# Optimization experiments

Hardware: AMD Instinct MI355X
Metric: run time of the kernel (lower is better)

The kernel has to match this reference:

```python
import jax, jax.numpy as jnp
import numpy as np

B, S, H, NH = 4, 2048, 768, 12
HD = H // NH

def _ln(x, g, b, eps=1e-5):
    m = jnp.mean(x, -1, keepdims=True)
    v = jnp.mean((x - m) ** 2, -1, keepdims=True)
    return (x - m) * jax.lax.rsqrt(v + eps) * g + b

def setup_inputs() -> dict:
    key = jax.random.key(0)
    ks = jax.random.split(key, 16)
    s = 0.02
    return {
        "x": jax.random.normal(ks[0], (B, S, H), jnp.float32),
        "prev_state": jax.random.normal(ks[1], (B, S, H), jnp.float32),
        "mask": jax.random.randint(ks[2], (B,), 0, 2).astype(bool),
        # depthwise conv1d (groups=H, k=3): torch weight [H, 1, 3] == OIH
        "conv_dw_w": jax.random.normal(ks[3], (H, 1, 3), jnp.float32) * s,
        "conv_dw_b": jnp.zeros((H,), jnp.float32),
        # pointwise conv1d (k=1) stored as [out, in]
        "conv_pw_w": jax.random.normal(ks[4], (H, H), jnp.float32) * s,
        "conv_pw_b": jnp.zeros((H,), jnp.float32),
        "cn_g": jnp.ones((H,), jnp.float32), "cn_b": jnp.zeros((H,), jnp.float32),
        "Wq": jax.random.normal(ks[5], (H, H), jnp.float32) * s, "bq": jnp.zeros((H,), jnp.float32),
        "Wk": jax.random.normal(ks[6], (H, H), jnp.float32) * s, "bk": jnp.zeros((H,), jnp.float32),
        "Wv": jax.random.normal(ks[7], (H, H), jnp.float32) * s, "bv": jnp.zeros((H,), jnp.float32),
        "Wo": jax.random.normal(ks[8], (H, H), jnp.float32) * s, "bo": jnp.zeros((H,), jnp.float32),
        "pn_g": jnp.ones((H,), jnp.float32), "pn_b": jnp.zeros((H,), jnp.float32),
        "Wpost": jax.random.normal(ks[9], (H, H), jnp.float32) * s, "bpost": jnp.zeros((H,), jnp.float32),
        "Wg": jax.random.normal(ks[10], (1, 2 * H), jnp.float32) * s, "bg": jnp.zeros((1,), jnp.float32),
    }

def reference(x, prev_state, mask, conv_dw_w, conv_dw_b, conv_pw_w, conv_pw_b,
              cn_g, cn_b, Wq, bq, Wk, bk, Wv, bv, Wo, bo,
              pn_g, pn_b, Wpost, bpost, Wg, bg):
    # ---- bridge: depthwise conv (k=3) -> pointwise conv (k=1) -> GELU -> LN ----
    mem_t = prev_state.transpose(0, 2, 1)  # [B, H, S]
    dw = jax.lax.conv_general_dilated(
        mem_t, conv_dw_w, window_strides=(1,), padding=[(1, 1)],
        feature_group_count=H, dimension_numbers=("NCH", "OIH", "NCH")) + conv_dw_b[None, :, None]
    pw = jnp.einsum("bhs,oh->bos", dw, conv_pw_w) + conv_pw_b[None, :, None]
    bridged = jax.nn.gelu(pw, approximate=False).transpose(0, 2, 1)  # [B, S, H]
    bridged = _ln(bridged, cn_g, cn_b)
    # ---- cross attention: q from x, k/v from bridged memory (nope, non-causal) ----
    q = (jnp.einsum("bsh,oh->bso", x, Wq) + bq).reshape(B, S, NH, HD)
    k = (jnp.einsum("bsh,oh->bso", bridged, Wk) + bk).reshape(B, S, NH, HD)
    v = (jnp.einsum("bsh,oh->bso", bridged, Wv) + bv).reshape(B, S, NH, HD)
    scores = jnp.einsum("bqnd,bknd->bnqk", q, k) / np.float32(np.sqrt(HD))
    attn = jax.nn.softmax(scores, axis=-1)
    ao = jnp.einsum("bnqk,bknd->bqnd", attn, v).reshape(B, S, H)
    ao = jnp.einsum("bsh,oh->bso", ao, Wo) + bo
    # ---- post-attn norm, linear, gate, scatter-add back under mask ----
    inj = _ln(ao, pn_g, pn_b)
    inj = jnp.einsum("bsh,oh->bso", inj, Wpost) + bpost
    gate = jax.nn.sigmoid(jnp.einsum("bsh,oh->bso", jnp.concatenate([x, bridged], -1), Wg) + bg)
    gated = gate * jnp.tanh(inj)
    mf = mask.astype(x.dtype)[:, None, None]  # batch-row select == masked scatter-add
    out = x + mf * gated
    # masked MSE aux loss (only over selected rows, as in the original)
    denom = jnp.maximum(mask.sum(), 1).astype(x.dtype) * np.float32(S * H)
    aux = jnp.sum(mf * (bridged - x) ** 2) / denom
    return out, aux
```

## Files before the change

kernel.cpp:

```cpp
#include <hip/hip_runtime.h>
#include <math.h>

#define B_ 4
#define S_ 2048
#define H_ 768
#define NH_ 12
#define HD_ 64
#define BSH (B_ * S_ * H_)
#define NROWS (B_ * S_)
#define WSZ (H_ * H_)

typedef __attribute__((ext_vector_type(8))) short bf16x8;
typedef __attribute__((ext_vector_type(4))) short s16x4;
typedef __attribute__((ext_vector_type(4))) float f32x4;
typedef __attribute__((ext_vector_type(2))) unsigned u32x2;
typedef __attribute__((ext_vector_type(4))) unsigned u32x4;

__device__ __forceinline__ short f2bf(float f) {
  union { float f; unsigned u; } x; x.f = f;
  unsigned r = x.u + 0x7FFF + ((x.u >> 16) & 1);
  return (short)(r >> 16);
}
__device__ __forceinline__ float bf2f(short s) {
  union { unsigned u; float f; } x;
  x.u = ((unsigned)(unsigned short)s) << 16;
  return x.f;
}
__device__ __forceinline__ unsigned bfpack(float lo, float hi) {
  union { float f; unsigned u; } a, b; a.f = lo; b.f = hi;
  return __builtin_amdgcn_perm(b.u, a.u, 0x07060302);
}

__device__ __forceinline__ void plswap32(unsigned& a, unsigned& b) {
#if __has_builtin(__builtin_amdgcn_permlane32_swap)
  u32x2 r = __builtin_amdgcn_permlane32_swap(a, b, false, false);
  a = r.x; b = r.y;
#else
  asm volatile("v_permlane32_swap_b32 %0, %1" : "+v"(a), "+v"(b));
#endif
}
__device__ __forceinline__ void plswap16(unsigned& a, unsigned& b) {
#if __has_builtin(__builtin_amdgcn_permlane16_swap)
  u32x2 r = __builtin_amdgcn_permlane16_swap(a, b, false, false);
  a = r.x; b = r.y;
#else
  asm volatile("v_permlane16_swap_b32 %0, %1" : "+v"(a), "+v"(b));
#endif
}

typedef __attribute__((address_space(1))) const unsigned int g_u32;
typedef __attribute__((address_space(3))) unsigned int l_u32;
__device__ __forceinline__ void gload16(const void* g, void* l) {
  __builtin_amdgcn_global_load_lds((g_u32*)g, (l_u32*)l, 16, 0, 0);
}

__global__ __launch_bounds__(256) void cvt_x_k(const float* __restrict__ src,
                                               short* __restrict__ dst) {
  int i = (blockIdx.x * 256 + threadIdx.x) * 4;
  float4 v = *(const float4*)(src + i);
  s16x4 o = {f2bf(v.x), f2bf(v.y), f2bf(v.z), f2bf(v.w)};
  *(s16x4*)(dst + i) = o;
}

__global__ __launch_bounds__(256) void cvt6_k(const float* w0, const float* w1,
                                              const float* w2, const float* w3,
                                              const float* w4, const float* w5,
                                              short* __restrict__ dst) {
  int i = (blockIdx.x * 256 + threadIdx.x) * 4;
  int m = i / WSZ;
  int off = i - m * WSZ;
  const float* s = m == 0 ? w0 : m == 1 ? w1 : m == 2 ? w2 : m == 3 ? w3 : m == 4 ? w4 : w5;
  float sc = (m == 1) ? 0.1803368802f : 1.0f;
  float4 v = *(const float4*)(s + off);
  s16x4 o = {f2bf(v.x * sc), f2bf(v.y * sc), f2bf(v.z * sc), f2bf(v.w * sc)};
  *(s16x4*)(dst + i) = o;
}

__global__ __launch_bounds__(192) void dwconv_k(const float* __restrict__ prev,
                                                const float* __restrict__ w3,
                                                const float* __restrict__ bias,
                                                short* __restrict__ out) {
  int row = blockIdx.x;
  int s = row & (S_ - 1);
  int h = threadIdx.x * 4;
  size_t base = (size_t)row * H_ + h;
  float4 c = *(const float4*)(prev + base);
  float4 wa = *(const float4*)(w3 + h * 3);
  float4 wb = *(const float4*)(w3 + h * 3 + 4);
  float4 wc = *(const float4*)(w3 + h * 3 + 8);
  float4 bi = *(const float4*)(bias + h);
  float4 acc;
  acc.x = bi.x + c.x * wa.y;
  acc.y = bi.y + c.y * wb.x;
  acc.z = bi.z + c.z * wb.w;
  acc.w = bi.w + c.w * wc.z;
  if (s > 0) {
    float4 l = *(const float4*)(prev + base - H_);
    acc.x += l.x * wa.x; acc.y += l.y * wa.w; acc.z += l.z * wb.z; acc.w += l.w * wc.y;
  }
  if (s < S_ - 1) {
    float4 r = *(const float4*)(prev + base + H_);
    acc.x += r.x * wa.z; acc.y += r.y * wb.y; acc.z += r.z * wc.x; acc.w += r.w * wc.w;
  }
  s16x4 o = {f2bf(acc.x), f2bf(acc.y), f2bf(acc.z), f2bf(acc.w)};
  *(s16x4*)(out + base) = o;
}

struct GemmJob {
  const short* A; const short* W; const float* bias; short* C; int act; int tout;
  float bscale;
};

__global__ __launch_bounds__(256) void gemm_bf2(GemmJob j0, GemmJob j1, GemmJob j2) {
  int d = blockIdx.x;
  int z = d / 384, r5 = d - z * 384;
  GemmJob j = z == 0 ? j0 : (z == 1 ? j1 : j2);
  int xcd = r5 & 7, s5 = r5 >> 3;
  int nx = s5 % 6, ny = xcd + 8 * (s5 / 6);
  __shared__ short As[128 * 64];
  __shared__ short Ws[128 * 64];
  int tid = threadIdx.x, lane = tid & 63, w = tid >> 6;
  int wr = w >> 1, wc = w & 1, lm = lane & 15, lq = lane >> 4;
  int m0 = ny * 128, n0 = nx * 128;
  int srow = lane >> 3;
  int skc = (lane & 7) * 8;
  const short* gA = j.A + (size_t)(m0 + w * 32 + srow) * H_ + skc;
  const short* gW = j.W + (size_t)(n0 + w * 32 + srow) * H_ + skc;
  short* lA = As + w * 2048;
  short* lW = Ws + w * 2048;

  f32x4 acc[4][4];
#pragma unroll
  for (int i = 0; i < 4; ++i)
#pragma unroll
    for (int jj = 0; jj < 4; ++jj) acc[i][jj] = (f32x4){0.f, 0.f, 0.f, 0.f};

  for (int kt = 0; kt < H_; kt += 64) {
    __syncthreads();
#pragma unroll
    for (int c = 0; c < 4; ++c) {
      gload16(gA + kt + (size_t)(c * 8) * H_, lA + c * 512);
      gload16(gW + kt + (size_t)(c * 8) * H_, lW + c * 512);
    }
    __syncthreads();
#pragma unroll
    for (int kk = 0; kk < 2; ++kk) {
      bf16x8 af[4], wf[4];
#pragma unroll
      for (int i = 0; i < 4; ++i)
        af[i] = *(const bf16x8*)&As[(wr * 64 + i * 16 + lm) * 64 + kk * 32 + lq * 8];
#pragma unroll
      for (int jj = 0; jj < 4; ++jj)
        wf[jj] = *(const bf16x8*)&Ws[(wc * 64 + jj * 16 + lm) * 64 + kk * 32 + lq * 8];
#pragma unroll
      for (int i = 0; i < 4; ++i)
#pragma unroll
        for (int jj = 0; jj < 4; ++jj)
          acc[i][jj] = __builtin_amdgcn_mfma_f32_16x16x32_bf16(af[i], wf[jj], acc[i][jj], 0, 0, 0);
    }
  }

  if (!j.tout) {
#pragma unroll
    for (int jj = 0; jj < 4; ++jj) {
      int col = n0 + wc * 64 + jj * 16 + lm;
      float bn = j.bias[col] * j.bscale;
#pragma unroll
      for (int i = 0; i < 4; ++i) {
        int mrow = m0 + wr * 64 + i * 16 + lq * 4;
#pragma unroll
        for (int r = 0; r < 4; ++r) {
          float cv = acc[i][jj][r] + bn;
          if (j.act) cv = 0.5f * cv * (1.0f + erff(cv * 0.70710678118f));
          j.C[(size_t)(mrow + r) * H_ + col] = f2bf(cv);
        }
      }
    }
  } else {
    int b = m0 >> 11;
    int sb = (m0 & (S_ - 1)) + wr * 64;
#pragma unroll
    for (int jj = 0; jj < 4; ++jj) {
      int col = n0 + wc * 64 + jj * 16 + lm;
      float bn = j.bias[col] * j.bscale;
      short* cp = j.C + ((size_t)(b * H_ + col)) * S_;
#pragma unroll
      for (int i = 0; i < 4; ++i) {
        int s = sb + i * 16 + lq * 4;
        s16x4 pk = {f2bf(acc[i][jj][0] + bn), f2bf(acc[i][jj][1] + bn),
                    f2bf(acc[i][jj][2] + bn), f2bf(acc[i][jj][3] + bn)};
        *(s16x4*)(cp + s) = pk;
      }
    }
  }
}

__global__ __launch_bounds__(256) void gemm_n64(const short* __restrict__ A,
                                                const short* __restrict__ W,
                                                const float* __restrict__ bias,
                                                short* __restrict__ C, int act) {
  int d = blockIdx.x;
  int xcd = d & 7, s5 = d >> 3;
  int nx = s5 % 12, ny = xcd + 8 * (s5 / 12);
  __shared__ short As[128 * 64];
  __shared__ short Ws[64 * 64];
  int tid = threadIdx.x, lane = tid & 63, w = tid >> 6;
  int wm = w >> 1, wn = w & 1, lm = lane & 15, lq = lane >> 4;
  int m0 = ny * 128, n0 = nx * 64;
  const short* gA = A + (size_t)(m0 + w * 32 + (lane >> 3)) * H_ + (lane & 7) * 8;
  const short* gW = W + (size_t)(n0 + w * 16 + (lane >> 3)) * H_ + (lane & 7) * 8;
  short* lA = As + w * 2048;
  short* lW = Ws + w * 1024;

  f32x4 acc[4][2];
#pragma unroll
  for (int i = 0; i < 4; ++i)
#pragma unroll
    for (int jj = 0; jj < 2; ++jj) acc[i][jj] = (f32x4){0.f, 0.f, 0.f, 0.f};

  for (int kt = 0; kt < H_; kt += 64) {
    __syncthreads();
#pragma unroll
    for (int c = 0; c < 4; ++c)
      gload16(gA + kt + (size_t)(c * 8) * H_, lA + c * 512);
#pragma unroll
    for (int c = 0; c < 2; ++c)
      gload16(gW + kt + (size_t)(c * 8) * H_, lW + c * 512);
    __syncthreads();
#pragma unroll
    for (int kk = 0; kk < 2; ++kk) {
      bf16x8 af[4], wf[2];
#pragma unroll
      for (int i = 0; i < 4; ++i)
        af[i] = *(const bf16x8*)&As[(wm * 64 + i * 16 + lm) * 64 + kk * 32 + lq * 8];
#pragma unroll
      for (int jj = 0; jj < 2; ++jj)
        wf[jj] = *(const bf16x8*)&Ws[(wn * 32 + jj * 16 + lm) * 64 + kk * 32 + lq * 8];
#pragma unroll
      for (int i = 0; i < 4; ++i)
#pragma unroll
        for (int jj = 0; jj < 2; ++jj)
          acc[i][jj] = __builtin_amdgcn_mfma_f32_16x16x32_bf16(af[i], wf[jj], acc[i][jj], 0, 0, 0);
    }
  }

#pragma unroll
  for (int jj = 0; jj < 2; ++jj) {
    int col = n0 + wn * 32 + jj * 16 + lm;
    float bn = bias[col];
#pragma unroll
    for (int i = 0; i < 4; ++i) {
      int mrow = m0 + wm * 64 + i * 16 + lq * 4;
#pragma unroll
      for (int r = 0; r < 4; ++r) {
        float cv = acc[i][jj][r] + bn;
        if (act) cv = 0.5f * cv * (1.0f + erff(cv * 0.70710678118f));
        C[(size_t)(mrow + r) * H_ + col] = f2bf(cv);
      }
    }
  }
}

__global__ __launch_bounds__(256) void ln_bf(const short* __restrict__ X,
                                             short* __restrict__ Y,
                                             const float* __restrict__ g,
                                             const float* __restrict__ bb) {
  int row = blockIdx.x;
  size_t base = (size_t)row * H_;
  int h0 = threadIdx.x, h1 = h0 + 256, h2 = h0 + 512;
  float x0 = bf2f(X[base + h0]), x1 = bf2f(X[base + h1]), x2 = bf2f(X[base + h2]);
  float s = x0 + x1 + x2;
  float s2 = x0 * x0 + x1 * x1 + x2 * x2;
  for (int off = 32; off > 0; off >>= 1) {
    s += __shfl_down(s, off);
    s2 += __shfl_down(s2, off);
  }
  __shared__ float sa[4], sq[4], st[2];
  int wid = threadIdx.x >> 6, lane = threadIdx.x & 63;
  if (lane == 0) { sa[wid] = s; sq[wid] = s2; }
  __syncthreads();
  if (threadIdx.x == 0) {
    float ts = sa[0] + sa[1] + sa[2] + sa[3];
    float ts2 = sq[0] + sq[1] + sq[2] + sq[3];
    float mean = ts * (1.0f / H_);
    float var = ts2 * (1.0f / H_) - mean * mean;
    st[0] = mean;
    st[1] = rsqrtf(var + 1e-5f);
  }
  __syncthreads();
  float mean = st[0], rstd = st[1];
  Y[base + h0] = f2bf((x0 - mean) * rstd * g[h0] + bb[h0]);
  Y[base + h1] = f2bf((x1 - mean) * rstd * g[h1] + bb[h1]);
  Y[base + h2] = f2bf((x2 - mean) * rstd * g[h2] + bb[h2]);
}

__global__ __launch_bounds__(256) void attn7_k(const short* __restrict__ qb,
                                               const short* __restrict__ kb,
                                               const short* __restrict__ vtb,
                                               short* __restrict__ aob) {
  __shared__ short Ks[2][64 * 64];
  __shared__ short Vt[2][64 * 64];
  int tid = threadIdx.x, lane = tid & 63, w = tid >> 6;
  int lm = lane & 15, lq = lane >> 4;
  int lm7 = lm & 7;
  int dd = blockIdx.x;
  int xcd = dd & 7, slot = dd >> 3;
  int g = xcd + 8 * (slot >> 4);
  int qx = slot & 15;
  int b = g / NH_, n = g - b * NH_;
  int q0 = qx * 128;
  int hoff = n * HD_;

  int rb8 = (lq ^ lm7) << 3;
  int rb8x = rb8 ^ 32;

  bf16x8 qf[2][2];
#pragma unroll
  for (int qg = 0; qg < 2; ++qg) {
    const short* qrow = qb + ((size_t)(b * S_ + q0 + w * 32 + qg * 16 + lm)) * H_ + hoff;
    qf[qg][0] = *(const bf16x8*)(qrow + lq * 8);
    qf[qg][1] = *(const bf16x8*)(qrow + 32 + lq * 8);
  }

  bf16x8 onef = {0x3F80, 0x3F80, 0x3F80, 0x3F80, 0x3F80, 0x3F80, 0x3F80, 0x3F80};
  f32x4 ls[2];
  ls[0] = (f32x4){0.f, 0.f, 0.f, 0.f};
  ls[1] = (f32x4){0.f, 0.f, 0.f, 0.f};

  f32x4 o[4][2];
#pragma unroll
  for (int i = 0; i < 4; ++i)
#pragma unroll
    for (int qg = 0; qg < 2; ++qg) o[i][qg] = (f32x4){0.f, 0.f, 0.f, 0.f};

  int r0 = tid >> 2;
  int c0 = (tid & 3) * 16;
  int sl = (tid & 3) * 2;
  int sw0 = r0 * 64 + ((sl ^ (r0 & 7)) << 3);
  int sw1 = r0 * 64 + (((sl ^ 1) ^ (r0 & 7)) << 3);
  const short* kg = kb + ((size_t)(b * S_)) * H_ + hoff;
  const short* vg = vtb + ((size_t)(b * H_ + hoff)) * S_;

  bf16x8 kv0 = *(const bf16x8*)(kg + (size_t)r0 * H_ + c0);
  bf16x8 kv1 = *(const bf16x8*)(kg + (size_t)r0 * H_ + c0 + 8);
  bf16x8 vv0 = *(const bf16x8*)(vg + (size_t)r0 * S_ + c0);
  bf16x8 vv1 = *(const bf16x8*)(vg + (size_t)r0 * S_ + c0 + 8);

  for (int kt = 0, pb = 0; kt < S_; kt += 64, pb ^= 1) {
    short* Kw = &Ks[pb][0];
    short* Vw = &Vt[pb][0];
    *(bf16x8*)&Kw[sw0] = kv0;
    *(bf16x8*)&Kw[sw1] = kv1;
    *(bf16x8*)&Vw[sw0] = vv0;
    *(bf16x8*)&Vw[sw1] = vv1;
    __syncthreads();
    if (kt + 64 < S_) {
      kv0 = *(const bf16x8*)(kg + (size_t)(kt + 64 + r0) * H_ + c0);
      kv1 = *(const bf16x8*)(kg + (size_t)(kt + 64 + r0) * H_ + c0 + 8);
      vv0 = *(const bf16x8*)(vg + (size_t)r0 * S_ + kt + 64 + c0);
      vv1 = *(const bf16x8*)(vg + (size_t)r0 * S_ + kt + 64 + c0 + 8);
    }

    f32x4 st[4][2];
    __builtin_amdgcn_s_setprio(1);
#pragma unroll
    for (int ni = 0; ni < 4; ++ni) {
      int krow = (ni * 16 + lm) * 64;
      bf16x8 ka0 = *(const bf16x8*)&Kw[krow + rb8];
      bf16x8 ka1 = *(const bf16x8*)&Kw[krow + rb8x];
#pragma unroll
      for (int qg = 0; qg < 2; ++qg) {
        f32x4 z = (f32x4){0.f, 0.f, 0.f, 0.f};
        z = __builtin_amdgcn_mfma_f32_16x16x32_bf16(ka0, qf[qg][0], z, 0, 0, 0);
        st[ni][qg] = __builtin_amdgcn_mfma_f32_16x16x32_bf16(ka1, qf[qg][1], z, 0, 0, 0);
      }
    }
    __builtin_amdgcn_s_setprio(0);

    bf16x8 pf[2][2];
#pragma unroll
    for (int qg = 0; qg < 2; ++qg) {
      unsigned pw0, pw1, pw2, pw3, pw4, pw5, pw6, pw7;
      {
        float p0 = exp2f(st[0][qg][0]), p1 = exp2f(st[0][qg][1]);
        float p2 = exp2f(st[0][qg][2]), p3 = exp2f(st[0][qg][3]);
        pw0 = bfpack(p0, p1); pw1 = bfpack(p2, p3);
      }
      {
        float p0 = exp2f(st[1][qg][0]), p1 = exp2f(st[1][qg][1]);
        float p2 = exp2f(st[1][qg][2]), p3 = exp2f(st[1][qg][3]);
        pw2 = bfpack(p0, p1); pw3 = bfpack(p2, p3);
      }
      {
        float p0 = exp2f(st[2][qg][0]), p1 = exp2f(st[2][qg][1]);
        float p2 = exp2f(st[2][qg][2]), p3 = exp2f(st[2][qg][3]);
        pw4 = bfpack(p0, p1); pw5 = bfpack(p2, p3);
      }
      {
        float p0 = exp2f(st[3][qg][0]), p1 = exp2f(st[3][qg][1]);
        float p2 = exp2f(st[3][qg][2]), p3 = exp2f(st[3][qg][3]);
        pw6 = bfpack(p0, p1); pw7 = bfpack(p2, p3);
      }
      plswap32(pw0, pw2); plswap16(pw0, pw2);
      plswap32(pw1, pw3); plswap16(pw1, pw3);
      plswap32(pw4, pw6); plswap16(pw4, pw6);
      plswap32(pw5, pw7); plswap16(pw5, pw7);
      union { u32x4 u; bf16x8 v; } c0u, c1u;
      c0u.u = (u32x4){pw0, pw1, pw2, pw3};
      c1u.u = (u32x4){pw4, pw5, pw6, pw7};
      pf[qg][0] = c0u.v;
      pf[qg][1] = c1u.v;
    }

    __builtin_amdgcn_s_setprio(1);
#pragma unroll
    for (int qg = 0; qg < 2; ++qg) {
      ls[qg] = __builtin_amdgcn_mfma_f32_16x16x32_bf16(onef, pf[qg][0], ls[qg], 0, 0, 0);
      ls[qg] = __builtin_amdgcn_mfma_f32_16x16x32_bf16(onef, pf[qg][1], ls[qg], 0, 0, 0);
    }
#pragma unroll
    for (int nd = 0; nd < 4; ++nd) {
      int vrow = (nd * 16 + lm) * 64;
      bf16x8 va0 = *(const bf16x8*)&Vw[vrow + rb8];
      bf16x8 va1 = *(const bf16x8*)&Vw[vrow + rb8x];
#pragma unroll
      for (int qg = 0; qg < 2; ++qg) {
        o[nd][qg] = __builtin_amdgcn_mfma_f32_16x16x32_bf16(va0, pf[qg][0], o[nd][qg], 0, 0, 0);
        o[nd][qg] = __builtin_amdgcn_mfma_f32_16x16x32_bf16(va1, pf[qg][1], o[nd][qg], 0, 0, 0);
      }
    }
    __builtin_amdgcn_s_setprio(0);
  }

#pragma unroll
  for (int qg = 0; qg < 2; ++qg) {
    float inv = 1.0f / ls[qg][0];
    short* orow = aob + ((size_t)(b * S_ + q0 + w * 32 + qg * 16 + lm)) * H_ + hoff;
#pragma unroll
    for (int nd = 0; nd < 4; ++nd) {
      s16x4 pk = {f2bf(o[nd][qg][0] * inv), f2bf(o[nd][qg][1] * inv),
                  f2bf(o[nd][qg][2] * inv), f2bf(o[nd][qg][3] * inv)};
      *(s16x4*)(orow + nd * 16 + lq * 4) = pk;
    }
  }
}

__global__ __launch_bounds__(192) void gate_out_k(const float* __restrict__ x,
                                                  const short* __restrict__ br,
                                                  const short* __restrict__ inj,
                                                  const int* __restrict__ mask,
                                                  const float* __restrict__ Wg,
                                                  const float* __restrict__ bg,
                                                  float* __restrict__ out,
                                                  float* __restrict__ paux) {
  int row = blockIdx.x;
  int b = row >> 11;
  size_t base = (size_t)row * H_;
  int h = threadIdx.x * 4;
  float4 xv = *(const float4*)(x + base + h);
  s16x4 brv = *(const s16x4*)(br + base + h);
  s16x4 inv = *(const s16x4*)(inj + base + h);
  float4 wg0 = *(const float4*)(Wg + h);
  float4 wg1 = *(const float4*)(Wg + H_ + h);
  float b0 = bf2f(brv.x), b1 = bf2f(brv.y), b2 = bf2f(brv.z), b3 = bf2f(brv.w);
  float dot = xv.x * wg0.x + xv.y * wg0.y + xv.z * wg0.z + xv.w * wg0.w
            + b0 * wg1.x + b1 * wg1.y + b2 * wg1.z + b3 * wg1.w;
  float d0 = b0 - xv.x, d1 = b1 - xv.y, d2 = b2 - xv.z, d3 = b3 - xv.w;
  float aux = d0 * d0 + d1 * d1 + d2 * d2 + d3 * d3;
  for (int off = 32; off > 0; off >>= 1) {
    dot += __shfl_down(dot, off);
    aux += __shfl_down(aux, off);
  }
  __shared__ float sd[3], sx[3], gsh[2];
  int wid = threadIdx.x >> 6, lane = threadIdx.x & 63;
  if (lane == 0) { sd[wid] = dot; sx[wid] = aux; }
  __syncthreads();
  if (threadIdx.x == 0) {
    float td = sd[0] + sd[1] + sd[2];
    float ta = sx[0] + sx[1] + sx[2];
    gsh[0] = 1.0f / (1.0f + expf(-(td + bg[0])));
    gsh[1] = ta;
  }
  __syncthreads();
  float mf = (mask[b] != 0) ? 1.0f : 0.0f;
  float gm = gsh[0] * mf;
  float v0 = bf2f(inv.x), v1 = bf2f(inv.y), v2 = bf2f(inv.z), v3 = bf2f(inv.w);
  float e0 = __expf(2.f * v0), e1 = __expf(2.f * v1), e2 = __expf(2.f * v2), e3 = __expf(2.f * v3);
  float4 ov;
  ov.x = xv.x + gm * ((e0 - 1.f) / (e0 + 1.f));
  ov.y = xv.y + gm * ((e1 - 1.f) / (e1 + 1.f));
  ov.z = xv.z + gm * ((e2 - 1.f) / (e2 + 1.f));
  ov.w = xv.w + gm * ((e3 - 1.f) / (e3 + 1.f));
  *(float4*)(out + base + h) = ov;
  if (threadIdx.x == 0) paux[row] = mf * gsh[1];
}

__global__ __launch_bounds__(256) void aux_reduce_k(const float* __restrict__ paux,
                                                    const int* __restrict__ mask,
                                                    float* __restrict__ outp) {
  float s = 0.f;
  for (int i = threadIdx.x; i < NROWS; i += 256) s += paux[i];
  for (int off = 32; off > 0; off >>= 1) s += __shfl_down(s, off);
  __shared__ float sw[4];
  int wid = threadIdx.x >> 6, lane = threadIdx.x & 63;
  if (lane == 0) sw[wid] = s;
  __syncthreads();
  if (threadIdx.x == 0) {
    float t = sw[0] + sw[1] + sw[2] + sw[3];
    int nm = (mask[0] != 0) + (mask[1] != 0) + (mask[2] != 0) + (mask[3] != 0);
    if (nm < 1) nm = 1;
    outp[0] = t / ((float)nm * (float)(S_ * H_));
  }
}

extern "C" void kernel_launch(void* const* d_in, const int* in_sizes, int n_in,
                              void* d_out, int out_size, void* d_ws, size_t ws_size,
                              hipStream_t stream) {
  const float* x     = (const float*)d_in[0];
  const float* prev  = (const float*)d_in[1];
  const int*   mask  = (const int*)d_in[2];
  const float* dw_w  = (const float*)d_in[3];
  const float* dw_b  = (const float*)d_in[4];
  const float* pw_w  = (const float*)d_in[5];
  const float* pw_b  = (const float*)d_in[6];
  const float* cn_g  = (const float*)d_in[7];
  const float* cn_b  = (const float*)d_in[8];
  const float* Wq    = (const float*)d_in[9];
  const float* bq    = (const float*)d_in[10];
  const float* Wk    = (const float*)d_in[11];
  const float* bk    = (const float*)d_in[12];
  const float* Wv    = (const float*)d_in[13];
  const float* bv    = (const float*)d_in[14];
  const float* Wo    = (const float*)d_in[15];
  const float* bo    = (const float*)d_in[16];
  const float* pn_g  = (const float*)d_in[17];
  const float* pn_b  = (const float*)d_in[18];
  const float* Wpost = (const float*)d_in[19];
  const float* bpost = (const float*)d_in[20];
  const float* Wg    = (const float*)d_in[21];
  const float* bg    = (const float*)d_in[22];
  float* out = (float*)d_out;

  short* B0 = (short*)d_ws;
  short* B1 = B0 + BSH;
  short* B2 = B1 + BSH;
  short* B3 = B2 + BSH;
  short* B4 = B3 + BSH;
  short* B5 = B4 + BSH;
  short* WW = B5 + BSH;
  float* paux = (float*)(WW + 6 * WSZ);

  const float C1 = 0.1803368802f;

  GemmJob jq = {B0, WW + WSZ,     bq, B1, 0, 0, C1};
  GemmJob jk = {B3, WW + 2 * WSZ, bk, B4, 0, 0, 1.0f};
  GemmJob jv = {B3, WW + 3 * WSZ, bv, B5, 0, 1, 1.0f};

  cvt6_k<<<6 * WSZ / 1024, 256, 0, stream>>>(pw_w, Wq, Wk, Wv, Wo, Wpost, WW);
  cvt_x_k<<<BSH / 1024, 256, 0, stream>>>(x, B0);
  dwconv_k<<<NROWS, 192, 0, stream>>>(prev, dw_w, dw_b, B1);
  gemm_n64<<<768, 256, 0, stream>>>(B1, WW, pw_b, B2, 1);
  ln_bf<<<NROWS, 256, 0, stream>>>(B2, B3, cn_g, cn_b);
  gemm_bf2<<<1152, 256, 0, stream>>>(jq, jk, jv);
  attn7_k<<<768, 256, 0, stream>>>(B1, B4, B5, B2);
  gemm_n64<<<768, 256, 0, stream>>>(B2, WW + 4 * WSZ, bo, B4, 0);
  ln_bf<<<NROWS, 256, 0, stream>>>(B4, B4, pn_g, pn_b);
  gemm_n64<<<768, 256, 0, stream>>>(B4, WW + 5 * WSZ, bpost, B5, 0);
  gate_out_k<<<NROWS, 192, 0, stream>>>(x, B3, B5, mask, Wg, bg, out, paux);
  aux_reduce_k<<<1, 256, 0, stream>>>(paux, mask, out + BSH);
}
```

Baseline: 391.3 us.

## Load attention K/V tiles directly to LDS and use raw exp2 intrinsic

The attention kernel now uses gload16, which appears to be a direct global-to-LDS load helper, to prefetch the next K and V tiles into the alternate shared buffer. This replaces the old path of loading into registers and then storing to LDS, and relies on the XOR-swizzled lane addressing to preserve the LDS layout. It also swaps exp2f for the hardware v_exp_f32 intrinsic in the softmax, dropping the range-handling code that exp2f adds. The risks are that only one barrier per iteration now guards the asynchronous LDS writes against readers of the other buffer, and that the raw intrinsic handles denormals and edge cases less carefully.

```diff
diff --git a/kernel.cpp b/kernel.cpp
--- a/kernel.cpp
+++ b/kernel.cpp
@@ -29,6 +29,16 @@
 __device__ __forceinline__ unsigned bfpack(float lo, float hi) {
   union { float f; unsigned u; } a, b; a.f = lo; b.f = hi;
   return __builtin_amdgcn_perm(b.u, a.u, 0x07060302);
+}
+
+__device__ __forceinline__ float fexp2(float x) {
+#if __has_builtin(__builtin_amdgcn_exp2f)
+  return __builtin_amdgcn_exp2f(x);
+#else
+  float r;
+  asm("v_exp_f32 %0, %1" : "=v"(r) : "v"(x));
+  return r;
+#endif
 }
 
 __device__ __forceinline__ void plswap32(unsigned& a, unsigned& b) {
@@ -294,7 +304,7 @@
   Y[base + h2] = f2bf((x2 - mean) * rstd * g[h2] + bb[h2]);
 }
 
-__global__ __launch_bounds__(256) void attn7_k(const short* __restrict__ qb,
+__global__ __launch_bounds__(256) void attn8_k(const short* __restrict__ qb,
                                                const short* __restrict__ kb,
                                                const short* __restrict__ vtb,
                                                short* __restrict__ aob) {
@@ -333,33 +343,29 @@
 #pragma unroll
     for (int qg = 0; qg < 2; ++qg) o[i][qg] = (f32x4){0.f, 0.f, 0.f, 0.f};
 
-  int r0 = tid >> 2;
-  int c0 = (tid & 3) * 16;
-  int sl = (tid & 3) * 2;
-  int sw0 = r0 * 64 + ((sl ^ (r0 & 7)) << 3);
-  int sw1 = r0 * 64 + (((sl ^ 1) ^ (r0 & 7)) << 3);
-  const short* kg = kb + ((size_t)(b * S_)) * H_ + hoff;
-  const short* vg = vtb + ((size_t)(b * H_ + hoff)) * S_;
-
-  bf16x8 kv0 = *(const bf16x8*)(kg + (size_t)r0 * H_ + c0);
-  bf16x8 kv1 = *(const bf16x8*)(kg + (size_t)r0 * H_ + c0 + 8);
-  bf16x8 vv0 = *(const bf16x8*)(vg + (size_t)r0 * S_ + c0);
-  bf16x8 vv1 = *(const bf16x8*)(vg + (size_t)r0 * S_ + c0 + 8);
+  int jl = ((lane & 7) ^ (lane >> 3)) * 8;
+  int rr = w * 16 + (lane >> 3);
+  const short* kgl = kb + ((size_t)(b * S_ + rr)) * H_ + hoff + jl;
+  const short* vgl = vtb + ((size_t)(b * H_ + hoff + rr)) * S_ + jl;
+  int lbase = w * 1024;
+
+#pragma unroll
+  for (int c = 0; c < 2; ++c) {
+    gload16(kgl + (size_t)(c * 8) * H_, &Ks[0][lbase + c * 512]);
+    gload16(vgl + (size_t)(c * 8) * S_, &Vt[0][lbase + c * 512]);
+  }
 
   for (int kt = 0, pb = 0; kt < S_; kt += 64, pb ^= 1) {
-    short* Kw = &Ks[pb][0];
-    short* Vw = &Vt[pb][0];
-    *(bf16x8*)&Kw[sw0] = kv0;
-    *(bf16x8*)&Kw[sw1] = kv1;
-    *(bf16x8*)&Vw[sw0] = vv0;
-    *(bf16x8*)&Vw[sw1] = vv1;
     __syncthreads();
     if (kt + 64 < S_) {
-      kv0 = *(const bf16x8*)(kg + (size_t)(kt + 64 + r0) * H_ + c0);
-      kv1 = *(const bf16x8*)(kg + (size_t)(kt + 64 + r0) * H_ + c0 + 8);
-      vv0 = *(const bf16x8*)(vg + (size_t)r0 * S_ + kt + 64 + c0);
-      vv1 = *(const bf16x8*)(vg + (size_t)r0 * S_ + kt + 64 + c0 + 8);
-    }
+#pragma unroll
+      for (int c = 0; c < 2; ++c) {
+        gload16(kgl + (size_t)(kt + 64 + c * 8) * H_, &Ks[pb ^ 1][lbase + c * 512]);
+        gload16(vgl + (size_t)(c * 8) * S_ + (kt + 64), &Vt[pb ^ 1][lbase + c * 512]);
+      }
+    }
+    const short* Kw = &Ks[pb][0];
+    const short* Vw = &Vt[pb][0];
 
     f32x4 st[4][2];
     __builtin_amdgcn_s_setprio(1);
@@ -382,23 +388,23 @@
     for (int qg = 0; qg < 2; ++qg) {
       unsigned pw0, pw1, pw2, pw3, pw4, pw5, pw6, pw7;
       {
-        float p0 = exp2f(st[0][qg][0]), p1 = exp2f(st[0][qg][1]);
-        float p2 = exp2f(st[0][qg][2]), p3 = exp2f(st[0][qg][3]);
+        float p0 = fexp2(st[0][qg][0]), p1 = fexp2(st[0][qg][1]);
+        float p2 = fexp2(st[0][qg][2]), p3 = fexp2(st[0][qg][3]);
         pw0 = bfpack(p0, p1); pw1 = bfpack(p2, p3);
       }
       {
-        float p0 = exp2f(st[1][qg][0]), p1 = exp2f(st[1][qg][1]);
-        float p2 = exp2f(st[1][qg][2]), p3 = exp2f(st[1][qg][3]);
+        float p0 = fexp2(st[1][qg][0]), p1 = fexp2(st[1][qg][1]);
+        float p2 = fexp2(st[1][qg][2]), p3 = fexp2(st[1][qg][3]);
         pw2 = bfpack(p0, p1); pw3 = bfpack(p2, p3);
       }
       {
-        float p0 = exp2f(st[2][qg][0]), p1 = exp2f(st[2][qg][1]);
-        float p2 = exp2f(st[2][qg][2]), p3 = exp2f(st[2][qg][3]);
+        float p0 = fexp2(st[2][qg][0]), p1 = fexp2(st[2][qg][1]);
+        float p2 = fexp2(st[2][qg][2]), p3 = fexp2(st[2][qg][3]);
         pw4 = bfpack(p0, p1); pw5 = bfpack(p2, p3);
       }
       {
-        float p0 = exp2f(st[3][qg][0]), p1 = exp2f(st[3][qg][1]);
-        float p2 = exp2f(st[3][qg][2]), p3 = exp2f(st[3][qg][3]);
+        float p0 = fexp2(st[3][qg][0]), p1 = fexp2(st[3][qg][1]);
+        float p2 = fexp2(st[3][qg][2]), p3 = fexp2(st[3][qg][3]);
         pw6 = bfpack(p0, p1); pw7 = bfpack(p2, p3);
       }
       plswap32(pw0, pw2); plswap16(pw0, pw2);
@@ -562,7 +568,7 @@
   gemm_n64<<<768, 256, 0, stream>>>(B1, WW, pw_b, B2, 1);
   ln_bf<<<NROWS, 256, 0, stream>>>(B2, B3, cn_g, cn_b);
   gemm_bf2<<<1152, 256, 0, stream>>>(jq, jk, jv);
-  attn7_k<<<768, 256, 0, stream>>>(B1, B4, B5, B2);
+  attn8_k<<<768, 256, 0, stream>>>(B1, B4, B5, B2);
   gemm_n64<<<768, 256, 0, stream>>>(B2, WW + 4 * WSZ, bo, B4, 0);
   ln_bf<<<NROWS, 256, 0, stream>>>(B4, B4, pn_g, pn_b);
   gemm_n64<<<768, 256, 0, stream>>>(B4, WW + 5 * WSZ, bpost, B5, 0);
```

Result: faster. 372.3 us (-4.9%).
